# Performance work log

Hardware: AMD Instinct MI355X
Metric: run time of the kernel (lower is better)

Reference implementation:

```python
import jax, jax.numpy as jnp
import numpy as np
import math

B, T, C = 4, 2048, 2048
HQ, HKV = 16, 4
HD = C // HQ          # 128
REP = HQ // HKV       # 4
EPS = 1e-6


def _rope_tables(seq_len, dim):
    inv_freq = 1.0 / (10000.0 ** (np.arange(0, dim, 2, dtype=np.float32) / dim))
    t = np.arange(seq_len, dtype=np.float32)
    freqs = np.einsum('i,j->ij', t, inv_freq)  # [T, dim/2]
    return jnp.asarray(np.cos(freqs)), jnp.asarray(np.sin(freqs))


def setup_inputs() -> dict:
    key = jax.random.key(0)
    ks = jax.random.split(key, 10)
    s = 0.02
    cos, sin = _rope_tables(T, HD)
    return {
        'x': jax.random.normal(ks[0], (B, T, C), jnp.float32),
        'Wq': jax.random.normal(ks[1], (C, C), jnp.float32) * s,
        'bq': jnp.zeros((C,), jnp.float32),
        'Wk': jax.random.normal(ks[2], (HD * HKV, C), jnp.float32) * s,
        'bk': jnp.zeros((HD * HKV,), jnp.float32),
        'Wv': jax.random.normal(ks[3], (HD * HKV, C), jnp.float32) * s,
        'bv': jnp.zeros((HD * HKV,), jnp.float32),
        'qn_w': jnp.ones((HD,), jnp.float32),
        'kn_w': jnp.ones((HD,), jnp.float32),
        'Wg': jax.random.normal(ks[4], (HD, HD), jnp.float32) * s,
        'bg': jnp.zeros((HD,), jnp.float32),
        'Wo': jax.random.normal(ks[5], (C, C), jnp.float32) * s,
        'bo': jnp.zeros((C,), jnp.float32),
        'cos': cos,
        'sin': sin,
    }


def _apply_rope(x, cos, sin):
    # x: [B,T,H,HD]; cos/sin: [T,HD/2]
    c = cos[None, :, None, :]
    s = sin[None, :, None, :]
    x1, x2 = x[..., ::2], x[..., 1::2]
    return jnp.concatenate([x1 * c - x2 * s, x1 * s + x2 * c], axis=-1)


def _rmsnorm(x, w):
    norm = jnp.mean(x * x, axis=-1, keepdims=True)
    return w * (x * jax.lax.rsqrt(norm + EPS))


def reference(x, Wq, bq, Wk, bk, Wv, bv, qn_w, kn_w, Wg, bg, Wo, bo, cos, sin):
    Bsz, Tlen, _ = x.shape
    q = (x @ Wq.T + bq).reshape(Bsz, Tlen, HQ, HD)
    k = (x @ Wk.T + bk).reshape(Bsz, Tlen, HKV, HD)
    v = (x @ Wv.T + bv).reshape(Bsz, Tlen, HKV, HD)

    q = _rmsnorm(_apply_rope(q, cos, sin), qn_w)
    k = _rmsnorm(_apply_rope(k, cos, sin), kn_w)

    # GQA without materializing repeated K/V: group q heads [B,T,HKV,REP,HD]
    # (repeat_interleave on kv-head dim matches this grouping exactly)
    q5 = q.reshape(Bsz, Tlen, HKV, REP, HD)
    scores = jnp.einsum('btkrd,bskd->bkrts', q5, k) / math.sqrt(HD)

    causal = jnp.tril(jnp.ones((Tlen, Tlen), bool))
    scores = jnp.where(causal, scores, -jnp.inf)
    probs = jax.nn.softmax(scores, axis=-1)

    out = jnp.einsum('bkrts,bskd->btkrd', probs, v).reshape(Bsz, Tlen, HQ, HD)
    gate = jax.nn.sigmoid(out @ Wg.T + bg)
    out = (out * gate).reshape(Bsz, Tlen, C)
    return out @ Wo.T + bo
```

## Files before the change

kernel.cpp:

```cpp
#include <hip/hip_runtime.h>
#include <hip/hip_bf16.h>
#include <math.h>

typedef __attribute__((ext_vector_type(8))) __bf16 bf16x8;
typedef __attribute__((ext_vector_type(4))) float f32x4;

__device__ __forceinline__ void stage16(const void* g, void* l) {
#if __has_builtin(__builtin_amdgcn_global_load_lds)
  __builtin_amdgcn_global_load_lds(
      (const __attribute__((address_space(1))) void*)g,
      (__attribute__((address_space(3))) void*)l, 16, 0, 0);
#else
  *(int4*)l = *(const int4*)g;
#endif
}

__device__ __forceinline__ float sigmoidf_(float x) {
  return 1.0f / (1.0f + __expf(-x));
}

__global__ __launch_bounds__(256) void f2b_kernel(const float* __restrict__ s,
                                                  __bf16* __restrict__ d, int n) {
  int i = (blockIdx.x * blockDim.x + threadIdx.x) * 4;
  if (i >= n) return;
  float4 v = *(const float4*)(s + i);
  union { __bf16 h[4]; int2 p; } u;
  u.h[0] = (__bf16)v.x; u.h[1] = (__bf16)v.y;
  u.h[2] = (__bf16)v.z; u.h[3] = (__bf16)v.w;
  *(int2*)(d + i) = u.p;
}

template <typename OutT>
__global__ __launch_bounds__(256) void gemm_bt(const __bf16* __restrict__ A,
                                               const __bf16* __restrict__ Bm,
                                               const float* __restrict__ bias,
                                               OutT* __restrict__ C,
                                               int M, int N, int K) {
  __shared__ __align__(16) __bf16 As[128 * 64];
  __shared__ __align__(16) __bf16 Bs[128 * 64];
  const int tid = threadIdx.x;
  const int lane = tid & 63;
  const int w = tid >> 6;
  const int wr = w >> 1, wc = w & 1;
  const int m0 = blockIdx.y * 128, n0 = blockIdx.x * 128;
  const int r = lane & 15;
  const int ks = (lane >> 4) * 8;

  f32x4 acc[4][4] = {};

  for (int k0 = 0; k0 < K; k0 += 64) {
#pragma unroll
    for (int i = 0; i < 4; ++i) {
      int c = i * 256 + tid;
      int row = c >> 3, c8 = (c & 7) * 8;
      stage16(A + (size_t)(m0 + row) * K + k0 + c8, &As[c * 8]);
      stage16(Bm + (size_t)(n0 + row) * K + k0 + c8, &Bs[c * 8]);
    }
    __syncthreads();
#pragma unroll
    for (int kk = 0; kk < 2; ++kk) {
      bf16x8 af[4], bfr[4];
#pragma unroll
      for (int mi = 0; mi < 4; ++mi)
        af[mi] = *(const bf16x8*)&As[(wr * 64 + mi * 16 + r) * 64 + kk * 32 + ks];
#pragma unroll
      for (int ni = 0; ni < 4; ++ni)
        bfr[ni] = *(const bf16x8*)&Bs[(wc * 64 + ni * 16 + r) * 64 + kk * 32 + ks];
#pragma unroll
      for (int mi = 0; mi < 4; ++mi)
#pragma unroll
        for (int ni = 0; ni < 4; ++ni)
          acc[mi][ni] = __builtin_amdgcn_mfma_f32_16x16x32_bf16(
              af[mi], bfr[ni], acc[mi][ni], 0, 0, 0);
    }
    __syncthreads();
  }

  const int rq = lane >> 4;
#pragma unroll
  for (int mi = 0; mi < 4; ++mi) {
#pragma unroll
    for (int ni = 0; ni < 4; ++ni) {
      int col = n0 + wc * 64 + ni * 16 + r;
      float bv = bias ? bias[col] : 0.0f;
#pragma unroll
      for (int j = 0; j < 4; ++j) {
        int row = m0 + wr * 64 + mi * 16 + rq * 4 + j;
        C[(size_t)row * N + col] = (OutT)(acc[mi][ni][j] + bv);
      }
    }
  }
}

template <typename OutT>
__global__ __launch_bounds__(512, 1) void gemm256(const __bf16* __restrict__ A,
                                                  const __bf16* __restrict__ Bm,
                                                  const float* __restrict__ bias,
                                                  OutT* __restrict__ C,
                                                  int M, int N, int K, int gx) {
  __shared__ __align__(16) __bf16 Sm[2][2][2][128 * 64];
  const int tid = threadIdx.x, lane = tid & 63, wid = tid >> 6;
  const int wm = wid >> 2, wn = wid & 3;
  const int r = lane & 15, g4 = lane >> 4;
  const int nwg = gridDim.x, qx = nwg >> 3;
  const int wg = (blockIdx.x & 7) * qx + (blockIdx.x >> 3);
  const int m0 = (wg / gx) * 256, n0 = (wg % gx) * 256;

  f32x4 acc[8][4] = {};
  const int NT = K >> 6;

#define STAGE_HALF(buf, which, half, kt)                                          \
  {                                                                               \
    const __bf16* sp_ = (which) ? Bm : A;                                         \
    const int base_ = ((which) ? n0 : m0) + (half) * 128;                         \
    const int k0_ = (kt) << 6;                                                    \
    __bf16* dp_ = &Sm[buf][which][half][0];                                       \
    _Pragma("unroll") for (int i_ = 0; i_ < 2; ++i_) {                            \
      int c_ = i_ * 512 + tid;                                                    \
      int row_ = c_ >> 3, slot_ = c_ & 7;                                         \
      stage16(sp_ + (size_t)(base_ + row_) * K + k0_ + ((slot_ ^ (row_ & 7)) << 3), \
              dp_ + c_ * 8);                                                      \
    }                                                                             \
  }
#define LDSW(base, row, kk) \
  (*(const bf16x8*)&(base)[(row) * 64 + ((((kk) * 4 + g4) ^ ((row) & 7)) << 3)])

  STAGE_HALF(0, 0, 0, 0) STAGE_HALF(0, 0, 1, 0) STAGE_HALF(0, 1, 0, 0) STAGE_HALF(0, 1, 1, 0)

  const int brow = (wn & 1) * 64;
  bf16x8 af[4][2], bfr[2][2];

  for (int kt = 0; kt < NT; ++kt) {
    const int cur = kt & 1, nxt = cur ^ 1;
    const bool more = (kt + 1) < NT;
    const __bf16* Ah = &Sm[cur][0][wm][0];
    const __bf16* Bh = &Sm[cur][1][wn >> 1][0];

    if (more) STAGE_HALF(nxt, 0, 0, kt + 1)
    if (more) { asm volatile("s_waitcnt vmcnt(2)" ::: "memory"); }
    else      { asm volatile("s_waitcnt vmcnt(0)" ::: "memory"); }
    __builtin_amdgcn_s_barrier();
    asm volatile("" ::: "memory");
#pragma unroll
    for (int m = 0; m < 4; ++m)
#pragma unroll
      for (int kk = 0; kk < 2; ++kk) af[m][kk] = LDSW(Ah, m * 16 + r, kk);
#pragma unroll
    for (int n = 0; n < 2; ++n)
#pragma unroll
      for (int kk = 0; kk < 2; ++kk) bfr[n][kk] = LDSW(Bh, brow + n * 16 + r, kk);
    asm volatile("s_waitcnt lgkmcnt(0)" ::: "memory");
    __builtin_amdgcn_sched_barrier(0);
    __builtin_amdgcn_s_setprio(1);
#pragma unroll
    for (int m = 0; m < 4; ++m)
#pragma unroll
      for (int n = 0; n < 2; ++n)
#pragma unroll
        for (int kk = 0; kk < 2; ++kk)
          acc[m][n] = __builtin_amdgcn_mfma_f32_16x16x32_bf16(af[m][kk], bfr[n][kk],
                                                              acc[m][n], 0, 0, 0);
    __builtin_amdgcn_s_setprio(0);
    __builtin_amdgcn_s_barrier();

#pragma unroll
    for (int n = 0; n < 2; ++n)
#pragma unroll
      for (int kk = 0; kk < 2; ++kk) bfr[n][kk] = LDSW(Bh, brow + (2 + n) * 16 + r, kk);
    if (more) STAGE_HALF(nxt, 0, 1, kt + 1)
    asm volatile("s_waitcnt lgkmcnt(0)" ::: "memory");
    __builtin_amdgcn_sched_barrier(0);
    __builtin_amdgcn_s_setprio(1);
#pragma unroll
    for (int m = 0; m < 4; ++m)
#pragma unroll
      for (int n = 0; n < 2; ++n)
#pragma unroll
        for (int kk = 0; kk < 2; ++kk)
          acc[m][2 + n] = __builtin_amdgcn_mfma_f32_16x16x32_bf16(af[m][kk], bfr[n][kk],
                                                                  acc[m][2 + n], 0, 0, 0);
    __builtin_amdgcn_s_setprio(0);
    __builtin_amdgcn_s_barrier();

#pragma unroll
    for (int m = 0; m < 4; ++m)
#pragma unroll
      for (int kk = 0; kk < 2; ++kk) af[m][kk] = LDSW(Ah, (4 + m) * 16 + r, kk);
#pragma unroll
    for (int n = 0; n < 2; ++n)
#pragma unroll
      for (int kk = 0; kk < 2; ++kk) bfr[n][kk] = LDSW(Bh, brow + n * 16 + r, kk);
    if (more) STAGE_HALF(nxt, 1, 0, kt + 1)
    asm volatile("s_waitcnt lgkmcnt(0)" ::: "memory");
    __builtin_amdgcn_sched_barrier(0);
    __builtin_amdgcn_s_setprio(1);
#pragma unroll
    for (int m = 0; m < 4; ++m)
#pragma unroll
      for (int n = 0; n < 2; ++n)
#pragma unroll
        for (int kk = 0; kk < 2; ++kk)
          acc[4 + m][n] = __builtin_amdgcn_mfma_f32_16x16x32_bf16(af[m][kk], bfr[n][kk],
                                                                  acc[4 + m][n], 0, 0, 0);
    __builtin_amdgcn_s_setprio(0);
    __builtin_amdgcn_s_barrier();

#pragma unroll
    for (int n = 0; n < 2; ++n)
#pragma unroll
      for (int kk = 0; kk < 2; ++kk) bfr[n][kk] = LDSW(Bh, brow + (2 + n) * 16 + r, kk);
    if (more) STAGE_HALF(nxt, 1, 1, kt + 1)
    asm volatile("s_waitcnt lgkmcnt(0)" ::: "memory");
    __builtin_amdgcn_sched_barrier(0);
    __builtin_amdgcn_s_setprio(1);
#pragma unroll
    for (int m = 0; m < 4; ++m)
#pragma unroll
      for (int n = 0; n < 2; ++n)
#pragma unroll
        for (int kk = 0; kk < 2; ++kk)
          acc[4 + m][2 + n] = __builtin_amdgcn_mfma_f32_16x16x32_bf16(af[m][kk], bfr[n][kk],
                                                                      acc[4 + m][2 + n], 0, 0, 0);
    __builtin_amdgcn_s_setprio(0);
    __builtin_amdgcn_s_barrier();
  }

  const int rq = lane >> 4;
#pragma unroll
  for (int m = 0; m < 8; ++m)
#pragma unroll
    for (int n = 0; n < 4; ++n) {
      int col = n0 + wn * 64 + n * 16 + r;
      float bv = bias ? bias[col] : 0.0f;
#pragma unroll
      for (int j = 0; j < 4; ++j) {
        int row = m0 + wm * 128 + m * 16 + rq * 4 + j;
        C[(size_t)row * N + col] = (OutT)(acc[m][n][j] + bv);
      }
    }
#undef STAGE_HALF
#undef LDSW
}

__global__ __launch_bounds__(256) void vtrans(const __bf16* __restrict__ Y,
                                              __bf16* __restrict__ VT) {
  __shared__ __bf16 tile[32][66];
  const int t0 = blockIdx.x * 64;
  const int d0 = blockIdx.y * 32;
  const int bh = blockIdx.z;
  const int b = bh >> 2, hv = bh & 3;
  const __bf16* src = Y + (size_t)b * 2048 * 3072 + 2560 + hv * 128 + d0;
  const int dd = threadIdx.x & 31, tt = threadIdx.x >> 5;
#pragma unroll
  for (int p = 0; p < 8; ++p) {
    int t = tt + p * 8;
    tile[dd][t] = src[(size_t)(t0 + t) * 3072 + dd];
  }
  __syncthreads();
  __bf16* dst = VT + ((size_t)bh * 128 + d0) * 2048 + t0;
  const int oc = threadIdx.x & 63, orr = threadIdx.x >> 6;
#pragma unroll
  for (int p = 0; p < 8; ++p) {
    int d = orr + p * 4;
    dst[(size_t)d * 2048 + oc] = tile[d][oc];
  }
}

__global__ __launch_bounds__(256) void rope_norm(const __bf16* __restrict__ Y,
                                                 const float* __restrict__ cosT,
                                                 const float* __restrict__ sinT,
                                                 const float* __restrict__ qn,
                                                 const float* __restrict__ kn,
                                                 __bf16* __restrict__ qat,
                                                 __bf16* __restrict__ kat) {
  const int tok = blockIdx.x;
  const int b = tok >> 11, t = tok & 2047;
  const int wv = threadIdx.x >> 6, l = threadIdx.x & 63;
  const __bf16* row = Y + (size_t)tok * 3072;
  const float c = cosT[t * 64 + l], s = sinT[t * 64 + l];
#pragma unroll
  for (int i = 0; i < 5; ++i) {
    const int h = wv + i * 4;
    const bool isq = h < 16;
    const int base = isq ? h * 128 : 2048 + (h - 16) * 128;
    union { uint32_t u; __bf16 h2[2]; } p;
    p.u = *(const uint32_t*)(row + base + 2 * l);
    float x1 = (float)p.h2[0], x2 = (float)p.h2[1];
    float v1 = x1 * c - x2 * s;
    float v2 = x1 * s + x2 * c;
    float ss = v1 * v1 + v2 * v2;
#pragma unroll
    for (int o = 32; o >= 1; o >>= 1) ss += __shfl_xor(ss, o, 64);
    float rms = rsqrtf(ss * (1.0f / 128.0f) + 1e-6f);
    float w1 = isq ? qn[l] : kn[l];
    float w2 = isq ? qn[64 + l] : kn[64 + l];
    size_t ob = isq ? (((size_t)b * 16 + h) * 2048 + t) * 128
                    : (((size_t)b * 4 + (h - 16)) * 2048 + t) * 128;
    __bf16* dst = isq ? qat : kat;
    dst[ob + l] = (__bf16)(w1 * v1 * rms);
    dst[ob + 64 + l] = (__bf16)(w2 * v2 * rms);
  }
}

__global__ __launch_bounds__(512, 4) void attn4(const __bf16* __restrict__ Q,
                                                const __bf16* __restrict__ Kg,
                                                const __bf16* __restrict__ VTg,
                                                __bf16* __restrict__ ab) {
  __shared__ __align__(16) __bf16 Kt[2][64 * 128];
  __shared__ __align__(16) __bf16 Vt[2][128 * 64];
  __shared__ __align__(16) __bf16 Ps[8 * 16 * 64];
  const int tid = threadIdx.x, lane = tid & 63, wv = tid >> 6;
  const int b = blockIdx.z, hq = blockIdx.y, hkv = hq >> 2;
  const int p = blockIdx.x;
  const __bf16* qp = Q + ((size_t)b * 16 + hq) * 2048 * 128;
  const __bf16* kp = Kg + ((size_t)b * 4 + hkv) * 2048 * 128;
  const __bf16* vp = VTg + ((size_t)b * 4 + hkv) * 128 * 2048;
  const int r = lane & 15, g4 = lane >> 4, ks = g4 * 8;
  const float SCALE = 0.08838834764831845f;

#define STAGE_TILE(bi, kv0)                                                  \
  {                                                                          \
    __bf16* Kb = &Kt[bi][0];                                                 \
    __bf16* Vb = &Vt[bi][0];                                                 \
    _Pragma("unroll") for (int i = 0; i < 2; ++i) {                          \
      int c = i * 512 + tid;                                                 \
      int row = c >> 4, slot = c & 15;                                       \
      int gco = ((slot ^ (row & 7)) << 3);                                   \
      stage16(kp + (size_t)((kv0) + row) * 128 + gco, &Kb[c * 8]);           \
    }                                                                        \
    _Pragma("unroll") for (int i = 0; i < 2; ++i) {                          \
      int c = i * 512 + tid;                                                 \
      int row = c >> 3, slot = c & 7;                                        \
      int gco = ((slot ^ (row & 7)) << 3);                                   \
      stage16(vp + (size_t)row * 2048 + (kv0) + gco, &Vb[c * 8]);            \
    }                                                                        \
  }

  for (int half = 0; half < 2; ++half) {
    const int qt = half == 0 ? (15 - p) : p;
    const int q0 = qt * 128 + wv * 16;

    bf16x8 qf[4];
#pragma unroll
    for (int kk = 0; kk < 4; ++kk)
      qf[kk] = *(const bf16x8*)(qp + (size_t)(q0 + r) * 128 + kk * 32 + ks);

    f32x4 Of[8] = {};
    float mrow[4] = {-1e30f, -1e30f, -1e30f, -1e30f};
    float lrow[4] = {0.f, 0.f, 0.f, 0.f};

    const int nt = 2 * qt + 2;
    STAGE_TILE(0, 0);
    int cur = 0;
    for (int t = 0; t < nt; ++t) {
      const int kv0 = t * 64;
      if (t + 1 < nt) {
        STAGE_TILE(cur ^ 1, (t + 1) * 64);
        asm volatile("s_waitcnt vmcnt(4)" ::: "memory");
      } else {
        asm volatile("s_waitcnt vmcnt(0)" ::: "memory");
      }
      __builtin_amdgcn_s_barrier();

      const __bf16* Kb = &Kt[cur][0];
      const __bf16* Vb = &Vt[cur][0];

      f32x4 s[4];
      __builtin_amdgcn_s_setprio(1);
#pragma unroll
      for (int kj = 0; kj < 4; ++kj) {
        f32x4 sa = {};
        int krow = kj * 16 + r;
#pragma unroll
        for (int kk = 0; kk < 4; ++kk) {
          int slot = (kk * 4 + g4) ^ (r & 7);
          bf16x8 kf = *(const bf16x8*)&Kb[krow * 128 + slot * 8];
          sa = __builtin_amdgcn_mfma_f32_16x16x32_bf16(qf[kk], kf, sa, 0, 0, 0);
        }
        s[kj] = sa;
      }
      __builtin_amdgcn_s_setprio(0);
#pragma unroll
      for (int kj = 0; kj < 4; ++kj)
#pragma unroll
        for (int j = 0; j < 4; ++j) s[kj][j] *= SCALE;
      if (kv0 + 63 > q0) {
#pragma unroll
        for (int kj = 0; kj < 4; ++kj)
#pragma unroll
          for (int j = 0; j < 4; ++j) {
            int kv = kv0 + kj * 16 + r;
            int qrow = q0 + g4 * 4 + j;
            if (kv > qrow) s[kj][j] = -1e30f;
          }
      }
      float tm[4], corr[4], rs[4];
#pragma unroll
      for (int j = 0; j < 4; ++j)
        tm[j] = fmaxf(fmaxf(s[0][j], s[1][j]), fmaxf(s[2][j], s[3][j]));
#pragma unroll
      for (int o = 8; o >= 1; o >>= 1)
#pragma unroll
        for (int j = 0; j < 4; ++j) tm[j] = fmaxf(tm[j], __shfl_xor(tm[j], o, 64));
#pragma unroll
      for (int j = 0; j < 4; ++j) {
        float mn = fmaxf(mrow[j], tm[j]);
        corr[j] = __expf(mrow[j] - mn);
        mrow[j] = mn;
        float acc = 0.f;
#pragma unroll
        for (int kj = 0; kj < 4; ++kj) { s[kj][j] = __expf(s[kj][j] - mn); acc += s[kj][j]; }
        rs[j] = acc;
      }
#pragma unroll
      for (int o = 8; o >= 1; o >>= 1)
#pragma unroll
        for (int j = 0; j < 4; ++j) rs[j] += __shfl_xor(rs[j], o, 64);
#pragma unroll
      for (int j = 0; j < 4; ++j) lrow[j] = lrow[j] * corr[j] + rs[j];
#pragma unroll
      for (int f = 0; f < 8; ++f)
#pragma unroll
        for (int j = 0; j < 4; ++j) Of[f][j] *= corr[j];

      __bf16* pw = &Ps[wv * 16 * 64];
#pragma unroll
      for (int kj = 0; kj < 4; ++kj)
#pragma unroll
        for (int j = 0; j < 4; ++j) {
          int qr = g4 * 4 + j;
          int kvl = kj * 16 + r;
          int sl = (kvl >> 3) ^ (qr & 7);
          pw[qr * 64 + sl * 8 + (kvl & 7)] = (__bf16)s[kj][j];
        }
      __builtin_amdgcn_s_setprio(1);
#pragma unroll
      for (int kvj = 0; kvj < 2; ++kvj) {
        int sl = (kvj * 4 + g4) ^ (r & 7);
        bf16x8 pa = *(const bf16x8*)&pw[r * 64 + sl * 8];
#pragma unroll
        for (int dn = 0; dn < 8; ++dn) {
          bf16x8 vb = *(const bf16x8*)&Vb[(dn * 16 + r) * 64 + sl * 8];
          Of[dn] = __builtin_amdgcn_mfma_f32_16x16x32_bf16(pa, vb, Of[dn], 0, 0, 0);
        }
      }
      __builtin_amdgcn_s_setprio(0);
      __builtin_amdgcn_s_barrier();
      cur ^= 1;
    }

    float inv[4];
#pragma unroll
    for (int j = 0; j < 4; ++j) inv[j] = 1.0f / lrow[j];
#pragma unroll
    for (int dn = 0; dn < 8; ++dn)
#pragma unroll
      for (int j = 0; j < 4; ++j) {
        int row = q0 + g4 * 4 + j;
        int d = dn * 16 + r;
        ab[(((size_t)b * 2048 + row) * 16 + hq) * 128 + d] = (__bf16)(Of[dn][j] * inv[j]);
      }
  }
#undef STAGE_TILE
}

__global__ __launch_bounds__(256) void gate_mul(const __bf16* __restrict__ ao,
                                                const __bf16* __restrict__ g,
                                                __bf16* __restrict__ og, int n) {
  int i = (blockIdx.x * blockDim.x + threadIdx.x) * 8;
  if (i >= n) return;
  bf16x8 a = *(const bf16x8*)(ao + i);
  bf16x8 gg = *(const bf16x8*)(g + i);
  bf16x8 o;
#pragma unroll
  for (int e = 0; e < 8; ++e)
    o[e] = (__bf16)((float)a[e] * sigmoidf_((float)gg[e]));
  *(bf16x8*)(og + i) = o;
}

extern "C" void kernel_launch(void* const* d_in, const int* in_sizes, int n_in,
                              void* d_out, int out_size, void* d_ws, size_t ws_size,
                              hipStream_t stream) {
  const float* x    = (const float*)d_in[0];
  const float* Wq   = (const float*)d_in[1];
  const float* bq   = (const float*)d_in[2];
  const float* Wk   = (const float*)d_in[3];
  const float* bk   = (const float*)d_in[4];
  const float* Wv   = (const float*)d_in[5];
  const float* bv   = (const float*)d_in[6];
  const float* qn   = (const float*)d_in[7];
  const float* kn   = (const float*)d_in[8];
  const float* Wg   = (const float*)d_in[9];
  const float* bg   = (const float*)d_in[10];
  const float* Wo   = (const float*)d_in[11];
  const float* bo   = (const float*)d_in[12];
  const float* cosT = (const float*)d_in[13];
  const float* sinT = (const float*)d_in[14];

  char* ws = (char*)d_ws;
  constexpr size_t OFF_WQKV = 0;
  constexpr size_t OFF_WO   = OFF_WQKV + 3072ull * 2048 * 2;
  constexpr size_t OFF_WG   = OFF_WO + 2048ull * 2048 * 2;
  constexpr size_t OFF_BQKV = OFF_WG + 128ull * 128 * 2;
  constexpr size_t OFF_XB   = OFF_BQKV + 16384;
  constexpr size_t OFF_Y    = OFF_XB + 8192ull * 2048 * 2;
  constexpr size_t OFF_QAT  = OFF_Y + 8192ull * 3072 * 2;
  constexpr size_t OFF_KAT  = OFF_QAT + 4ull * 16 * 2048 * 128 * 2;
  constexpr size_t OFF_VT   = OFF_KAT + 4ull * 4 * 2048 * 128 * 2;
  constexpr size_t OFF_AB   = OFF_VT + 4ull * 4 * 2048 * 128 * 2;

  __bf16* WQKVb = (__bf16*)(ws + OFF_WQKV);
  __bf16* WOb   = (__bf16*)(ws + OFF_WO);
  __bf16* WGb   = (__bf16*)(ws + OFF_WG);
  float*  BQKV  = (float*)(ws + OFF_BQKV);
  __bf16* XB    = (__bf16*)(ws + OFF_XB);
  __bf16* Y     = (__bf16*)(ws + OFF_Y);
  __bf16* QAT   = (__bf16*)(ws + OFF_QAT);
  __bf16* KAT   = (__bf16*)(ws + OFF_KAT);
  __bf16* VT    = (__bf16*)(ws + OFF_VT);
  __bf16* ABuf  = (__bf16*)(ws + OFF_AB);
  __bf16* Gbuf  = (__bf16*)(ws + OFF_Y);
  __bf16* OGB   = (__bf16*)(ws + OFF_XB);

  f2b_kernel<<<16384, 256, 0, stream>>>(x, XB, 16777216);
  f2b_kernel<<<4096, 256, 0, stream>>>(Wq, WQKVb, 4194304);
  f2b_kernel<<<1024, 256, 0, stream>>>(Wk, WQKVb + 2048ull * 2048, 1048576);
  f2b_kernel<<<1024, 256, 0, stream>>>(Wv, WQKVb + 2560ull * 2048, 1048576);
  f2b_kernel<<<4096, 256, 0, stream>>>(Wo, WOb, 4194304);
  f2b_kernel<<<16, 256, 0, stream>>>(Wg, WGb, 16384);
  hipMemcpyAsync(BQKV, bq, 2048 * 4, hipMemcpyDeviceToDevice, stream);
  hipMemcpyAsync(BQKV + 2048, bk, 512 * 4, hipMemcpyDeviceToDevice, stream);
  hipMemcpyAsync(BQKV + 2560, bv, 512 * 4, hipMemcpyDeviceToDevice, stream);

  gemm256<__bf16><<<384, 512, 0, stream>>>(XB, WQKVb, BQKV, Y, 8192, 3072, 2048, 12);

  rope_norm<<<8192, 256, 0, stream>>>(Y, cosT, sinT, qn, kn, QAT, KAT);
  vtrans<<<dim3(32, 4, 16), 256, 0, stream>>>(Y, VT);

  attn4<<<dim3(8, 16, 4), 512, 0, stream>>>(QAT, KAT, VT, ABuf);

  gemm_bt<__bf16><<<dim3(1, 1024), 256, 0, stream>>>(ABuf, WGb, bg, Gbuf, 131072, 128, 128);
  gate_mul<<<8192, 256, 0, stream>>>(ABuf, Gbuf, OGB, 16777216);

  gemm256<float><<<256, 512, 0, stream>>>(OGB, WOb, bo, (float*)d_out, 8192, 2048, 2048, 8);
}
```

Baseline: 454.5 us.

## Fuse gate GEMM with sigmoid multiply, remap attention blocks to XCDs, lazy rescale

Replaces the separate gate GEMM and gate_mul kernels with one fused kernel. It keeps Wg in LDS, computes the 128x128 gate projection per 64-row tile, and applies sigmoid and the multiply in the epilogue, so the intermediate gate tensor never round-trips through memory. The attention grid is flattened and remapped so that all query heads sharing a KV head land on the same XCD, which should improve L2 reuse of K/V. Online softmax now rescales O and l only when some row's max grows by more than 8, skipping most of the correction exponentials and multiplies. The cost is slightly looser numerical bounds on the exponentials and an uncoalesced scalar epilogue in the gate kernel.

```diff
diff --git a/kernel.cpp b/kernel.cpp
--- a/kernel.cpp
+++ b/kernel.cpp
@@ -28,68 +28,6 @@
   u.h[0] = (__bf16)v.x; u.h[1] = (__bf16)v.y;
   u.h[2] = (__bf16)v.z; u.h[3] = (__bf16)v.w;
   *(int2*)(d + i) = u.p;
-}
-
-template <typename OutT>
-__global__ __launch_bounds__(256) void gemm_bt(const __bf16* __restrict__ A,
-                                               const __bf16* __restrict__ Bm,
-                                               const float* __restrict__ bias,
-                                               OutT* __restrict__ C,
-                                               int M, int N, int K) {
-  __shared__ __align__(16) __bf16 As[128 * 64];
-  __shared__ __align__(16) __bf16 Bs[128 * 64];
-  const int tid = threadIdx.x;
-  const int lane = tid & 63;
-  const int w = tid >> 6;
-  const int wr = w >> 1, wc = w & 1;
-  const int m0 = blockIdx.y * 128, n0 = blockIdx.x * 128;
-  const int r = lane & 15;
-  const int ks = (lane >> 4) * 8;
-
-  f32x4 acc[4][4] = {};
-
-  for (int k0 = 0; k0 < K; k0 += 64) {
-#pragma unroll
-    for (int i = 0; i < 4; ++i) {
-      int c = i * 256 + tid;
-      int row = c >> 3, c8 = (c & 7) * 8;
-      stage16(A + (size_t)(m0 + row) * K + k0 + c8, &As[c * 8]);
-      stage16(Bm + (size_t)(n0 + row) * K + k0 + c8, &Bs[c * 8]);
-    }
-    __syncthreads();
-#pragma unroll
-    for (int kk = 0; kk < 2; ++kk) {
-      bf16x8 af[4], bfr[4];
-#pragma unroll
-      for (int mi = 0; mi < 4; ++mi)
-        af[mi] = *(const bf16x8*)&As[(wr * 64 + mi * 16 + r) * 64 + kk * 32 + ks];
-#pragma unroll
-      for (int ni = 0; ni < 4; ++ni)
-        bfr[ni] = *(const bf16x8*)&Bs[(wc * 64 + ni * 16 + r) * 64 + kk * 32 + ks];
-#pragma unroll
-      for (int mi = 0; mi < 4; ++mi)
-#pragma unroll
-        for (int ni = 0; ni < 4; ++ni)
-          acc[mi][ni] = __builtin_amdgcn_mfma_f32_16x16x32_bf16(
-              af[mi], bfr[ni], acc[mi][ni], 0, 0, 0);
-    }
-    __syncthreads();
-  }
-
-  const int rq = lane >> 4;
-#pragma unroll
-  for (int mi = 0; mi < 4; ++mi) {
-#pragma unroll
-    for (int ni = 0; ni < 4; ++ni) {
-      int col = n0 + wc * 64 + ni * 16 + r;
-      float bv = bias ? bias[col] : 0.0f;
-#pragma unroll
-      for (int j = 0; j < 4; ++j) {
-        int row = m0 + wr * 64 + mi * 16 + rq * 4 + j;
-        C[(size_t)row * N + col] = (OutT)(acc[mi][ni][j] + bv);
-      }
-    }
-  }
 }
 
 template <typename OutT>
@@ -302,7 +240,7 @@
   }
 }
 
-__global__ __launch_bounds__(512, 4) void attn4(const __bf16* __restrict__ Q,
+__global__ __launch_bounds__(512, 4) void attn5(const __bf16* __restrict__ Q,
                                                 const __bf16* __restrict__ Kg,
                                                 const __bf16* __restrict__ VTg,
                                                 __bf16* __restrict__ ab) {
@@ -310,8 +248,13 @@
   __shared__ __align__(16) __bf16 Vt[2][128 * 64];
   __shared__ __align__(16) __bf16 Ps[8 * 16 * 64];
   const int tid = threadIdx.x, lane = tid & 63, wv = tid >> 6;
-  const int b = blockIdx.z, hq = blockIdx.y, hkv = hq >> 2;
-  const int p = blockIdx.x;
+  const int L = blockIdx.x;
+  const int xcd = L & 7, slot = L >> 3;
+  const int group = xcd * 2 + (slot >> 5);
+  const int idx = slot & 31;
+  const int b = group >> 2, hkv = group & 3;
+  const int hq = hkv * 4 + (idx >> 3);
+  const int p = idx & 7;
   const __bf16* qp = Q + ((size_t)b * 16 + hq) * 2048 * 128;
   const __bf16* kp = Kg + ((size_t)b * 4 + hkv) * 2048 * 128;
   const __bf16* vp = VTg + ((size_t)b * 4 + hkv) * 128 * 2048;
@@ -324,14 +267,14 @@
     __bf16* Vb = &Vt[bi][0];                                                 \
     _Pragma("unroll") for (int i = 0; i < 2; ++i) {                          \
       int c = i * 512 + tid;                                                 \
-      int row = c >> 4, slot = c & 15;                                       \
-      int gco = ((slot ^ (row & 7)) << 3);                                   \
+      int row = c >> 4, slot_ = c & 15;                                      \
+      int gco = ((slot_ ^ (row & 7)) << 3);                                  \
       stage16(kp + (size_t)((kv0) + row) * 128 + gco, &Kb[c * 8]);           \
     }                                                                        \
     _Pragma("unroll") for (int i = 0; i < 2; ++i) {                          \
       int c = i * 512 + tid;                                                 \
-      int row = c >> 3, slot = c & 7;                                        \
-      int gco = ((slot ^ (row & 7)) << 3);                                   \
+      int row = c >> 3, slot_ = c & 7;                                       \
+      int gco = ((slot_ ^ (row & 7)) << 3);                                  \
       stage16(vp + (size_t)row * 2048 + (kv0) + gco, &Vb[c * 8]);            \
     }                                                                        \
   }
@@ -373,8 +316,8 @@
         int krow = kj * 16 + r;
 #pragma unroll
         for (int kk = 0; kk < 4; ++kk) {
-          int slot = (kk * 4 + g4) ^ (r & 7);
-          bf16x8 kf = *(const bf16x8*)&Kb[krow * 128 + slot * 8];
+          int slot_ = (kk * 4 + g4) ^ (r & 7);
+          bf16x8 kf = *(const bf16x8*)&Kb[krow * 128 + slot_ * 8];
           sa = __builtin_amdgcn_mfma_f32_16x16x32_bf16(qf[kk], kf, sa, 0, 0, 0);
         }
         s[kj] = sa;
@@ -394,7 +337,7 @@
             if (kv > qrow) s[kj][j] = -1e30f;
           }
       }
-      float tm[4], corr[4], rs[4];
+      float tm[4], rs[4];
 #pragma unroll
       for (int j = 0; j < 4; ++j)
         tm[j] = fmaxf(fmaxf(s[0][j], s[1][j]), fmaxf(s[2][j], s[3][j]));
@@ -402,14 +345,24 @@
       for (int o = 8; o >= 1; o >>= 1)
 #pragma unroll
         for (int j = 0; j < 4; ++j) tm[j] = fmaxf(tm[j], __shfl_xor(tm[j], o, 64));
+      float growth = fmaxf(fmaxf(tm[0] - mrow[0], tm[1] - mrow[1]),
+                           fmaxf(tm[2] - mrow[2], tm[3] - mrow[3]));
+      if (__any(growth > 8.0f)) {
+#pragma unroll
+        for (int j = 0; j < 4; ++j) {
+          float mn = fmaxf(mrow[j], tm[j]);
+          float corr = __expf(mrow[j] - mn);
+          mrow[j] = mn;
+          lrow[j] *= corr;
+#pragma unroll
+          for (int f = 0; f < 8; ++f) Of[f][j] *= corr;
+        }
+      }
 #pragma unroll
       for (int j = 0; j < 4; ++j) {
-        float mn = fmaxf(mrow[j], tm[j]);
-        corr[j] = __expf(mrow[j] - mn);
-        mrow[j] = mn;
         float acc = 0.f;
 #pragma unroll
-        for (int kj = 0; kj < 4; ++kj) { s[kj][j] = __expf(s[kj][j] - mn); acc += s[kj][j]; }
+        for (int kj = 0; kj < 4; ++kj) { s[kj][j] = __expf(s[kj][j] - mrow[j]); acc += s[kj][j]; }
         rs[j] = acc;
       }
 #pragma unroll
@@ -417,11 +370,7 @@
 #pragma unroll
         for (int j = 0; j < 4; ++j) rs[j] += __shfl_xor(rs[j], o, 64);
 #pragma unroll
-      for (int j = 0; j < 4; ++j) lrow[j] = lrow[j] * corr[j] + rs[j];
-#pragma unroll
-      for (int f = 0; f < 8; ++f)
-#pragma unroll
-        for (int j = 0; j < 4; ++j) Of[f][j] *= corr[j];
+      for (int j = 0; j < 4; ++j) lrow[j] += rs[j];
 
       __bf16* pw = &Ps[wv * 16 * 64];
 #pragma unroll
@@ -464,18 +413,48 @@
 #undef STAGE_TILE
 }
 
-__global__ __launch_bounds__(256) void gate_mul(const __bf16* __restrict__ ao,
-                                                const __bf16* __restrict__ g,
-                                                __bf16* __restrict__ og, int n) {
-  int i = (blockIdx.x * blockDim.x + threadIdx.x) * 8;
-  if (i >= n) return;
-  bf16x8 a = *(const bf16x8*)(ao + i);
-  bf16x8 gg = *(const bf16x8*)(g + i);
-  bf16x8 o;
-#pragma unroll
-  for (int e = 0; e < 8; ++e)
-    o[e] = (__bf16)((float)a[e] * sigmoidf_((float)gg[e]));
-  *(bf16x8*)(og + i) = o;
+__global__ __launch_bounds__(256) void gate_fused(const __bf16* __restrict__ a,
+                                                  const __bf16* __restrict__ WgB,
+                                                  const float* __restrict__ bg,
+                                                  __bf16* __restrict__ og) {
+  __shared__ __align__(16) __bf16 Wl[128 * 128];
+  const int tid = threadIdx.x, lane = tid & 63, wv = tid >> 6;
+  const int r = lane & 15, g4 = lane >> 4, ks = g4 * 8;
+#pragma unroll
+  for (int i = 0; i < 8; ++i) {
+    int c = i * 256 + tid;
+    int row = c >> 4, slot = c & 15;
+    *(bf16x8*)&Wl[row * 128 + ((slot ^ (row & 7)) << 3)] =
+        *(const bf16x8*)&WgB[row * 128 + slot * 8];
+  }
+  __syncthreads();
+  const size_t r0 = (size_t)blockIdx.x * 64 + wv * 16;
+  bf16x8 af[4];
+#pragma unroll
+  for (int kk = 0; kk < 4; ++kk)
+    af[kk] = *(const bf16x8*)(a + (r0 + r) * 128 + kk * 32 + ks);
+  f32x4 acc[8] = {};
+#pragma unroll
+  for (int dn = 0; dn < 8; ++dn) {
+    int row = dn * 16 + r;
+#pragma unroll
+    for (int kk = 0; kk < 4; ++kk) {
+      bf16x8 bf_ = *(const bf16x8*)&Wl[row * 128 + (((kk * 4 + g4) ^ (row & 7)) << 3)];
+      acc[dn] = __builtin_amdgcn_mfma_f32_16x16x32_bf16(af[kk], bf_, acc[dn], 0, 0, 0);
+    }
+  }
+#pragma unroll
+  for (int dn = 0; dn < 8; ++dn) {
+    float bgv = bg[dn * 16 + r];
+#pragma unroll
+    for (int j = 0; j < 4; ++j) {
+      size_t row = r0 + g4 * 4 + j;
+      int col = dn * 16 + r;
+      float gv = sigmoidf_(acc[dn][j] + bgv);
+      float av = (float)a[row * 128 + col];
+      og[row * 128 + col] = (__bf16)(av * gv);
+    }
+  }
 }
 
 extern "C" void kernel_launch(void* const* d_in, const int* in_sizes, int n_in,
@@ -519,7 +498,6 @@
   __bf16* KAT   = (__bf16*)(ws + OFF_KAT);
   __bf16* VT    = (__bf16*)(ws + OFF_VT);
   __bf16* ABuf  = (__bf16*)(ws + OFF_AB);
-  __bf16* Gbuf  = (__bf16*)(ws + OFF_Y);
   __bf16* OGB   = (__bf16*)(ws + OFF_XB);
 
   f2b_kernel<<<16384, 256, 0, stream>>>(x, XB, 16777216);
@@ -537,10 +515,9 @@
   rope_norm<<<8192, 256, 0, stream>>>(Y, cosT, sinT, qn, kn, QAT, KAT);
   vtrans<<<dim3(32, 4, 16), 256, 0, stream>>>(Y, VT);
 
-  attn4<<<dim3(8, 16, 4), 512, 0, stream>>>(QAT, KAT, VT, ABuf);
-
-  gemm_bt<__bf16><<<dim3(1, 1024), 256, 0, stream>>>(ABuf, WGb, bg, Gbuf, 131072, 128, 128);
-  gate_mul<<<8192, 256, 0, stream>>>(ABuf, Gbuf, OGB, 16777216);
+  attn5<<<512, 512, 0, stream>>>(QAT, KAT, VT, ABuf);
+
+  gate_fused<<<2048, 256, 0, stream>>>(ABuf, WGb, bg, OGB);
 
   gemm256<float><<<256, 512, 0, stream>>>(OGB, WOb, bo, (float*)d_out, 8192, 2048, 2048, 8);
 }
```

New measurement: 438.4 us. -3.5%, faster.
